# Optimization experiments

Measured on AMD Instinct MI355X. Metric: run time of the kernel, lower is better.

The kernel has to match this reference:

```python
import jax, jax.numpy as jnp
import numpy as np

N = 100000
F_IN = 128
F_OUT = 128
NNZ = 1_600_000  # avg degree 16


def spmm(rows, cols, vals, X, n):
    """Sparse [n,n] (COO: rows, cols, vals) times dense X [n,d] -> [n,d]."""
    return jax.ops.segment_sum(vals[:, None] * X[cols], rows, num_segments=n)


def setup_inputs() -> dict:
    key = jax.random.key(0)
    ks = jax.random.split(key, 8)
    x = jax.random.normal(ks[0], (N, F_IN), dtype=jnp.float32)
    W = jax.random.normal(ks[1], (F_IN, F_OUT), dtype=jnp.float32) * 0.05
    kernel = jnp.ones((N, 1), dtype=jnp.float32)  # tf.ones_initializer
    phi0_rows = jax.random.randint(ks[2], (NNZ,), 0, N, dtype=jnp.int64)
    phi0_cols = jax.random.randint(ks[3], (NNZ,), 0, N, dtype=jnp.int64)
    phi0_vals = jax.random.uniform(ks[4], (NNZ,), dtype=jnp.float32)
    phi1_rows = jax.random.randint(ks[5], (NNZ,), 0, N, dtype=jnp.int64)
    phi1_cols = jax.random.randint(ks[6], (NNZ,), 0, N, dtype=jnp.int64)
    phi1_vals = jax.random.uniform(ks[7], (NNZ,), dtype=jnp.float32)
    return {
        "x": x, "W": W, "kernel": kernel,
        "phi0_rows": phi0_rows, "phi0_cols": phi0_cols, "phi0_vals": phi0_vals,
        "phi1_rows": phi1_rows, "phi1_cols": phi1_cols, "phi1_vals": phi1_vals,
    }


def reference(x, W, kernel, phi0_rows, phi0_cols, phi0_vals,
              phi1_rows, phi1_cols, phi1_vals):
    # X' = x @ W  (dense feature projection)
    X_prime = x @ W  # [N, F_OUT]
    # X'_t = phi0 @ X'  (SpMM with wavelet basis)
    X_t = spmm(phi0_rows, phi0_cols, phi0_vals, X_prime, N)
    # out = phi1 @ (kernel * X'_t)  (elementwise spectral scaling then SpMM)
    out = spmm(phi1_rows, phi1_cols, phi1_vals, kernel * X_t, N)
    return jax.nn.relu(out)
```

## Files before the change

kernel.cpp:

```cpp
#include <hip/hip_runtime.h>


constexpr int kN = 100000;
constexpr int kF = 128;
constexpr int kNNZ = 1600000;

constexpr int kBuckets = (kN + 255) / 256;
constexpr int kBucketCap = 4608;
constexpr int kChunk = 8192;
constexpr int kChunkBlocks = (kNNZ + kChunk - 1) / kChunk;
constexpr int kScatBlocks = 2 * kChunkBlocks;
constexpr int kGemmBlocks = (kN + 63) / 64;

typedef short bf16x8 __attribute__((ext_vector_type(8)));
typedef float f32x4 __attribute__((ext_vector_type(4)));
typedef unsigned short ushort4v __attribute__((ext_vector_type(4)));

__device__ __forceinline__ unsigned short f32_to_bf16(float f) {
    unsigned int u = __float_as_uint(f);
    u += 0x7fffu + ((u >> 16) & 1u);
    return (unsigned short)(u >> 16);
}
__device__ __forceinline__ float bf16_to_f32(unsigned short h) {
    return __uint_as_float((unsigned int)h << 16);
}

__global__ __launch_bounds__(256) void transpose_w(const float* __restrict__ W,
                                                   unsigned short* __restrict__ Wt,
                                                   int* __restrict__ g0,
                                                   int* __restrict__ g1) {
    const int t = threadIdx.x;
    const int e = blockIdx.x * 256 + t;
    const int n = e & 127, k = e >> 7;
    Wt[n * 128 + k] = f32_to_bf16(W[e]);
    if (blockIdx.x == 0) {
        for (int i = t; i < kBuckets; i += 256) {
            g0[i] = i * kBucketCap;
            g1[i] = i * kBucketCap;
        }
    }
}

__global__ __launch_bounds__(256) void fused_gemm_scatter(
    const float* __restrict__ x, const unsigned short* __restrict__ Wt,
    unsigned short* __restrict__ Xpb,
    const int* __restrict__ r0, const int* __restrict__ c0, const float* __restrict__ v0,
    const int* __restrict__ r1, const int* __restrict__ c1, const float* __restrict__ v1,
    int* __restrict__ gc0, int* __restrict__ gc1,
    unsigned long long* __restrict__ s0, unsigned long long* __restrict__ s1) {
    __shared__ __align__(16) char smem[64 * 128 * 2];
    const int t = threadIdx.x;

    if (blockIdx.x >= kScatBlocks) {
        unsigned short* xs = (unsigned short*)smem;
        const int rowBase = (blockIdx.x - kScatBlocks) * 64;

        {
            const int lrow = t >> 2;
            const int q = t & 3;
            int srow = rowBase + lrow;
            if (srow >= kN) srow = kN - 1;
            const float4* xr = (const float4*)(x + (size_t)srow * kF) + q * 8;
            #pragma unroll
            for (int i = 0; i < 8; ++i) {
                const float4 f = xr[i];
                ushort4v h;
                h.x = f32_to_bf16(f.x); h.y = f32_to_bf16(f.y);
                h.z = f32_to_bf16(f.z); h.w = f32_to_bf16(f.w);
                const int kidx = q * 32 + i * 4;
                *(ushort4v*)&xs[lrow * 128 + (kidx ^ ((lrow & 7) << 3))] = h;
            }
        }
        __syncthreads();

        const int w = t >> 6;
        const int l = t & 63;
        const int lr = l & 15;
        const int lq = l >> 4;

        f32x4 acc[8];
        #pragma unroll
        for (int n = 0; n < 8; ++n) acc[n] = (f32x4){0.f, 0.f, 0.f, 0.f};

        const int arow = w * 16 + lr;
        #pragma unroll
        for (int ks = 0; ks < 4; ++ks) {
            const int akidx = ks * 32 + lq * 8;
            const bf16x8 a = *(const bf16x8*)&xs[arow * 128 + (akidx ^ ((arow & 7) << 3))];
            #pragma unroll
            for (int n = 0; n < 8; ++n) {
                const int bn = n * 16 + lr;
                const bf16x8 b = *(const bf16x8*)(Wt + bn * 128 + akidx);
                acc[n] = __builtin_amdgcn_mfma_f32_16x16x32_bf16(a, b, acc[n], 0, 0, 0);
            }
        }

        #pragma unroll
        for (int j = 0; j < 4; ++j) {
            const int row = rowBase + w * 16 + lq * 4 + j;
            if (row < kN) {
                unsigned short* orow = Xpb + (size_t)row * kF + lr;
                #pragma unroll
                for (int n = 0; n < 8; ++n) orow[n * 16] = f32_to_bf16(acc[n][j]);
            }
        }
    } else {
        int* hist = (int*)smem;
        int* hbase = hist + kBuckets;
        const int b = blockIdx.x;
        const bool m1 = b >= kChunkBlocks;
        const int cb = m1 ? b - kChunkBlocks : b;
        const int* rows = m1 ? r1 : r0;
        const int* cols = m1 ? c1 : c0;
        const float* vals = m1 ? v1 : v0;
        int* gcur = m1 ? gc1 : gc0;
        unsigned long long* stg = m1 ? s1 : s0;

        for (int i = t; i < kBuckets; i += 256) hist[i] = 0;
        __syncthreads();

        const int base0 = cb * kChunk;
        for (int j = 0; j < kChunk; j += 256) {
            const int idx = base0 + j + t;
            if (idx < kNNZ) atomicAdd(&hist[rows[idx] >> 8], 1);
        }
        __syncthreads();

        for (int i = t; i < kBuckets; i += 256) {
            const int c = hist[i];
            hbase[i] = c ? atomicAdd(&gcur[i], c) : 0;
            hist[i] = 0;
        }
        __syncthreads();

        for (int j = 0; j < kChunk; j += 256) {
            const int idx = base0 + j + t;
            if (idx < kNNZ) {
                const int r = rows[idx];
                const int bk = r >> 8;
                const int pos = hbase[bk] + atomicAdd(&hist[bk], 1);
                const unsigned int key =
                    ((unsigned int)(r & 255) << 17) | (unsigned int)cols[idx];
                stg[pos] = ((unsigned long long)__float_as_uint(vals[idx]) << 32) | key;
            }
        }
    }
}

__global__ __launch_bounds__(256) void bucket_sort(
    const int* __restrict__ gc0, const int* __restrict__ gc1,
    unsigned long long* __restrict__ s0, unsigned long long* __restrict__ s1,
    int* __restrict__ rs0, int* __restrict__ re0,
    int* __restrict__ rs1, int* __restrict__ re1) {
    __shared__ unsigned long long recs[kBucketCap];
    __shared__ int hist[256];
    __shared__ int sc[256];
    __shared__ int cur[256];

    const int b = blockIdx.x;
    const bool m1 = b >= kBuckets;
    const int bk = m1 ? b - kBuckets : b;
    const int* gcur = m1 ? gc1 : gc0;
    unsigned long long* stg = m1 ? s1 : s0;
    int* rs = m1 ? rs1 : rs0;
    int* re = m1 ? re1 : re0;

    const int t = threadIdx.x;
    const int start = bk * kBucketCap;
    const int nrec = gcur[bk] - start;

    hist[t] = 0;
    __syncthreads();

    for (int i = t; i < nrec; i += 256) {
        const unsigned long long p = stg[start + i];
        recs[i] = p;
        atomicAdd(&hist[((unsigned int)p >> 17) & 255], 1);
    }
    __syncthreads();

    const int v = hist[t];
    sc[t] = v;
    __syncthreads();
    #pragma unroll
    for (int off = 1; off < 256; off <<= 1) {
        const int add = (t >= off) ? sc[t - off] : 0;
        __syncthreads();
        sc[t] += add;
        __syncthreads();
    }
    {
        const int ex = sc[t] - v;
        cur[t] = ex;
        const int row = bk * 256 + t;
        if (row < kN) {
            rs[row] = start + ex;
            re[row] = start + sc[t];
        }
    }
    __syncthreads();

    for (int i = t; i < nrec; i += 256) {
        const unsigned long long p = recs[i];
        const int lr = (int)(((unsigned int)p >> 17) & 255);
        const int pos = atomicAdd(&cur[lr], 1);
        stg[start + pos] = p;
    }
}

template <bool ROW_SCALE, bool RELU, bool OUT_BF16>
__global__ __launch_bounds__(256) void spmm_csr(const int* __restrict__ rs,
                                                const int* __restrict__ re,
                                                const unsigned long long* __restrict__ rec,
                                                const float* __restrict__ scale,
                                                const unsigned short* __restrict__ Xin,
                                                void* __restrict__ Xout) {
    const int tid = blockIdx.x * 256 + threadIdx.x;
    const int r = tid >> 5;
    const int lane = tid & 31;

    const int s = rs[r];
    const int e = re[r];

    float4 acc = make_float4(0.f, 0.f, 0.f, 0.f);

    for (int base = s; base < e; base += 32) {
        int cl = 0;
        float vl = 0.f;
        if (base + lane < e) {
            const unsigned long long p = rec[base + lane];
            cl = (int)((unsigned int)p & 0x1FFFF);
            vl = __uint_as_float((unsigned int)(p >> 32));
        }
        const int m4 = (min(32, e - base) + 3) & ~3;
        for (int j = 0; j < m4; j += 4) {
            const int c0 = __shfl(cl, j, 32);
            const int c1 = __shfl(cl, j + 1, 32);
            const int c2 = __shfl(cl, j + 2, 32);
            const int c3 = __shfl(cl, j + 3, 32);
            const float w0 = __shfl(vl, j, 32);
            const float w1 = __shfl(vl, j + 1, 32);
            const float w2 = __shfl(vl, j + 2, 32);
            const float w3 = __shfl(vl, j + 3, 32);
            const ushort4v x0 = *(const ushort4v*)(Xin + (size_t)c0 * kF + lane * 4);
            const ushort4v x1 = *(const ushort4v*)(Xin + (size_t)c1 * kF + lane * 4);
            const ushort4v x2 = *(const ushort4v*)(Xin + (size_t)c2 * kF + lane * 4);
            const ushort4v x3 = *(const ushort4v*)(Xin + (size_t)c3 * kF + lane * 4);
            acc.x = fmaf(w0, bf16_to_f32(x0.x), acc.x);
            acc.y = fmaf(w0, bf16_to_f32(x0.y), acc.y);
            acc.z = fmaf(w0, bf16_to_f32(x0.z), acc.z);
            acc.w = fmaf(w0, bf16_to_f32(x0.w), acc.w);
            acc.x = fmaf(w1, bf16_to_f32(x1.x), acc.x);
            acc.y = fmaf(w1, bf16_to_f32(x1.y), acc.y);
            acc.z = fmaf(w1, bf16_to_f32(x1.z), acc.z);
            acc.w = fmaf(w1, bf16_to_f32(x1.w), acc.w);
            acc.x = fmaf(w2, bf16_to_f32(x2.x), acc.x);
            acc.y = fmaf(w2, bf16_to_f32(x2.y), acc.y);
            acc.z = fmaf(w2, bf16_to_f32(x2.z), acc.z);
            acc.w = fmaf(w2, bf16_to_f32(x2.w), acc.w);
            acc.x = fmaf(w3, bf16_to_f32(x3.x), acc.x);
            acc.y = fmaf(w3, bf16_to_f32(x3.y), acc.y);
            acc.z = fmaf(w3, bf16_to_f32(x3.z), acc.z);
            acc.w = fmaf(w3, bf16_to_f32(x3.w), acc.w);
        }
    }
    if (ROW_SCALE) {
        const float k = scale[r];
        acc.x *= k; acc.y *= k; acc.z *= k; acc.w *= k;
    }
    if (RELU) {
        acc.x = fmaxf(acc.x, 0.f); acc.y = fmaxf(acc.y, 0.f);
        acc.z = fmaxf(acc.z, 0.f); acc.w = fmaxf(acc.w, 0.f);
    }
    if (OUT_BF16) {
        ushort4v o;
        o.x = f32_to_bf16(acc.x); o.y = f32_to_bf16(acc.y);
        o.z = f32_to_bf16(acc.z); o.w = f32_to_bf16(acc.w);
        *(ushort4v*)((unsigned short*)Xout + (size_t)r * kF + lane * 4) = o;
    } else {
        ((float4*)Xout)[(size_t)r * 32 + lane] = acc;
    }
}

extern "C" void kernel_launch(void* const* d_in, const int* in_sizes, int n_in,
                              void* d_out, int out_size, void* d_ws, size_t ws_size,
                              hipStream_t stream) {
    const float* x    = (const float*)d_in[0];
    const float* W    = (const float*)d_in[1];
    const float* kern = (const float*)d_in[2];
    const int*   p0r  = (const int*)d_in[3];
    const int*   p0c  = (const int*)d_in[4];
    const float* p0v  = (const float*)d_in[5];
    const int*   p1r  = (const int*)d_in[6];
    const int*   p1c  = (const int*)d_in[7];
    const float* p1v  = (const float*)d_in[8];
    float* out = (float*)d_out;

    char* w = (char*)d_ws;
    size_t off = 0;
    unsigned short* Xpb = (unsigned short*)(w + off); off += (size_t)kN * kF * 2;
    unsigned short* Xtb = (unsigned short*)(w + off); off += (size_t)kN * kF * 2;
    unsigned short* Wt = (unsigned short*)(w + off);  off += 128 * 128 * 2;
    int* gcur0 = (int*)(w + off);                     off += 2048;
    int* gcur1 = (int*)(w + off);                     off += 2048;
    int* rs0 = (int*)(w + off);                       off += (size_t)kN * 4;
    int* re0 = (int*)(w + off);                       off += (size_t)kN * 4;
    int* rs1 = (int*)(w + off);                       off += (size_t)kN * 4;
    int* re1 = (int*)(w + off);                       off += (size_t)kN * 4;
    unsigned long long* stg0 = (unsigned long long*)(w + off);
    off += (size_t)kBuckets * kBucketCap * 8;
    unsigned long long* stg1 = (unsigned long long*)(w + off);
    off += (size_t)kBuckets * kBucketCap * 8;

    const int rowBlocks = kN * 32 / 256;

    transpose_w<<<64, 256, 0, stream>>>(W, Wt, gcur0, gcur1);

    fused_gemm_scatter<<<kScatBlocks + kGemmBlocks, 256, 0, stream>>>(
        x, Wt, Xpb, p0r, p0c, p0v, p1r, p1c, p1v, gcur0, gcur1, stg0, stg1);

    bucket_sort<<<2 * kBuckets, 256, 0, stream>>>(gcur0, gcur1, stg0, stg1,
                                                  rs0, re0, rs1, re1);

    spmm_csr<true, false, true><<<rowBlocks, 256, 0, stream>>>(
        rs0, re0, stg0, kern, Xpb, Xtb);

    spmm_csr<false, true, false><<<rowBlocks, 256, 0, stream>>>(
        rs1, re1, stg1, nullptr, Xtb, out);
}
```

Baseline: 206.9 us.

## Fuse per-bucket row sort into SpMM kernels with 128-row buckets

Removes the separate bucket_sort kernel and the rs/re row-pointer arrays. Each SpMM block now sorts its 128-row bucket into shared memory and consumes the records directly from LDS, so the staging array is no longer written back and re-read. Buckets shrink from 256 to 128 rows and scatter chunks from 8192 to 4096 records, and the scatter pass caches row indices in shared memory so rows are read from global memory only once. In exchange, each wave processes 16 rows serially and there are fewer, larger SpMM blocks, which may lower parallelism and latency hiding.

```diff
diff --git a/kernel.cpp b/kernel.cpp
--- a/kernel.cpp
+++ b/kernel.cpp
@@ -5,9 +5,9 @@
 constexpr int kF = 128;
 constexpr int kNNZ = 1600000;
 
-constexpr int kBuckets = (kN + 255) / 256;
-constexpr int kBucketCap = 4608;
-constexpr int kChunk = 8192;
+constexpr int kBuckets = (kN + 127) / 128;
+constexpr int kBucketCap = 2432;
+constexpr int kChunk = 4096;
 constexpr int kChunkBlocks = (kNNZ + kChunk - 1) / kChunk;
 constexpr int kScatBlocks = 2 * kChunkBlocks;
 constexpr int kGemmBlocks = (kN + 63) / 64;
@@ -48,7 +48,7 @@
     const int* __restrict__ r1, const int* __restrict__ c1, const float* __restrict__ v1,
     int* __restrict__ gc0, int* __restrict__ gc1,
     unsigned long long* __restrict__ s0, unsigned long long* __restrict__ s1) {
-    __shared__ __align__(16) char smem[64 * 128 * 2];
+    __shared__ __align__(16) char smem[kChunk * 4 + 2 * kBuckets * 4];
     const int t = threadIdx.x;
 
     if (blockIdx.x >= kScatBlocks) {
@@ -105,7 +105,8 @@
             }
         }
     } else {
-        int* hist = (int*)smem;
+        int* rowsc = (int*)smem;
+        int* hist  = rowsc + kChunk;
         int* hbase = hist + kBuckets;
         const int b = blockIdx.x;
         const bool m1 = b >= kChunkBlocks;
@@ -122,7 +123,9 @@
         const int base0 = cb * kChunk;
         for (int j = 0; j < kChunk; j += 256) {
             const int idx = base0 + j + t;
-            if (idx < kNNZ) atomicAdd(&hist[rows[idx] >> 8], 1);
+            const int r = (idx < kNNZ) ? rows[idx] : -1;
+            rowsc[j + t] = r;
+            if (r >= 0) atomicAdd(&hist[r >> 7], 1);
         }
         __syncthreads();
 
@@ -135,117 +138,91 @@
 
         for (int j = 0; j < kChunk; j += 256) {
             const int idx = base0 + j + t;
-            if (idx < kNNZ) {
-                const int r = rows[idx];
-                const int bk = r >> 8;
+            const int r = rowsc[j + t];
+            if (r >= 0) {
+                const int bk = r >> 7;
                 const int pos = hbase[bk] + atomicAdd(&hist[bk], 1);
                 const unsigned int key =
-                    ((unsigned int)(r & 255) << 17) | (unsigned int)cols[idx];
+                    ((unsigned int)(r & 127) << 17) | (unsigned int)cols[idx];
                 stg[pos] = ((unsigned long long)__float_as_uint(vals[idx]) << 32) | key;
             }
         }
     }
 }
 
-__global__ __launch_bounds__(256) void bucket_sort(
-    const int* __restrict__ gc0, const int* __restrict__ gc1,
-    unsigned long long* __restrict__ s0, unsigned long long* __restrict__ s1,
-    int* __restrict__ rs0, int* __restrict__ re0,
-    int* __restrict__ rs1, int* __restrict__ re1) {
+template <bool ROW_SCALE, bool RELU, bool OUT_BF16>
+__global__ __launch_bounds__(256) void sort_spmm(const int* __restrict__ gcur,
+                                                 const unsigned long long* __restrict__ stg,
+                                                 const float* __restrict__ scale,
+                                                 const unsigned short* __restrict__ Xin,
+                                                 void* __restrict__ Xout) {
     __shared__ unsigned long long recs[kBucketCap];
-    __shared__ int hist[256];
-    __shared__ int sc[256];
-    __shared__ int cur[256];
-
-    const int b = blockIdx.x;
-    const bool m1 = b >= kBuckets;
-    const int bk = m1 ? b - kBuckets : b;
-    const int* gcur = m1 ? gc1 : gc0;
-    unsigned long long* stg = m1 ? s1 : s0;
-    int* rs = m1 ? rs1 : rs0;
-    int* re = m1 ? re1 : re0;
-
+    __shared__ int hist[128];
+    __shared__ int sc[128];
+    __shared__ int cur[128];
+
+    const int bk = blockIdx.x;
     const int t = threadIdx.x;
     const int start = bk * kBucketCap;
     const int nrec = gcur[bk] - start;
 
-    hist[t] = 0;
+    if (t < 128) hist[t] = 0;
+    __syncthreads();
+
+    for (int i = t; i < nrec; i += 256) {
+        const unsigned int lo = (unsigned int)stg[start + i];
+        atomicAdd(&hist[(lo >> 17) & 127], 1);
+    }
+    __syncthreads();
+
+    const int v = (t < 128) ? hist[t] : 0;
+    if (t < 128) sc[t] = v;
+    __syncthreads();
+    #pragma unroll
+    for (int off = 1; off < 128; off <<= 1) {
+        const int add = (t < 128 && t >= off) ? sc[t - off] : 0;
+        __syncthreads();
+        if (t < 128) sc[t] += add;
+        __syncthreads();
+    }
+    if (t < 128) cur[t] = sc[t] - v;
     __syncthreads();
 
     for (int i = t; i < nrec; i += 256) {
         const unsigned long long p = stg[start + i];
-        recs[i] = p;
-        atomicAdd(&hist[((unsigned int)p >> 17) & 255], 1);
-    }
-    __syncthreads();
-
-    const int v = hist[t];
-    sc[t] = v;
-    __syncthreads();
-    #pragma unroll
-    for (int off = 1; off < 256; off <<= 1) {
-        const int add = (t >= off) ? sc[t - off] : 0;
-        __syncthreads();
-        sc[t] += add;
-        __syncthreads();
-    }
-    {
-        const int ex = sc[t] - v;
-        cur[t] = ex;
-        const int row = bk * 256 + t;
-        if (row < kN) {
-            rs[row] = start + ex;
-            re[row] = start + sc[t];
-        }
-    }
-    __syncthreads();
-
-    for (int i = t; i < nrec; i += 256) {
-        const unsigned long long p = recs[i];
-        const int lr = (int)(((unsigned int)p >> 17) & 255);
-        const int pos = atomicAdd(&cur[lr], 1);
-        stg[start + pos] = p;
-    }
-}
-
-template <bool ROW_SCALE, bool RELU, bool OUT_BF16>
-__global__ __launch_bounds__(256) void spmm_csr(const int* __restrict__ rs,
-                                                const int* __restrict__ re,
-                                                const unsigned long long* __restrict__ rec,
-                                                const float* __restrict__ scale,
-                                                const unsigned short* __restrict__ Xin,
-                                                void* __restrict__ Xout) {
-    const int tid = blockIdx.x * 256 + threadIdx.x;
-    const int r = tid >> 5;
-    const int lane = tid & 31;
-
-    const int s = rs[r];
-    const int e = re[r];
-
-    float4 acc = make_float4(0.f, 0.f, 0.f, 0.f);
-
-    for (int base = s; base < e; base += 32) {
-        int cl = 0;
-        float vl = 0.f;
-        if (base + lane < e) {
-            const unsigned long long p = rec[base + lane];
-            cl = (int)((unsigned int)p & 0x1FFFF);
-            vl = __uint_as_float((unsigned int)(p >> 32));
-        }
-        const int m4 = (min(32, e - base) + 3) & ~3;
-        for (int j = 0; j < m4; j += 4) {
-            const int c0 = __shfl(cl, j, 32);
-            const int c1 = __shfl(cl, j + 1, 32);
-            const int c2 = __shfl(cl, j + 2, 32);
-            const int c3 = __shfl(cl, j + 3, 32);
-            const float w0 = __shfl(vl, j, 32);
-            const float w1 = __shfl(vl, j + 1, 32);
-            const float w2 = __shfl(vl, j + 2, 32);
-            const float w3 = __shfl(vl, j + 3, 32);
-            const ushort4v x0 = *(const ushort4v*)(Xin + (size_t)c0 * kF + lane * 4);
-            const ushort4v x1 = *(const ushort4v*)(Xin + (size_t)c1 * kF + lane * 4);
-            const ushort4v x2 = *(const ushort4v*)(Xin + (size_t)c2 * kF + lane * 4);
-            const ushort4v x3 = *(const ushort4v*)(Xin + (size_t)c3 * kF + lane * 4);
+        const int lr = (int)(((unsigned int)p >> 17) & 127);
+        recs[atomicAdd(&cur[lr], 1)] = p;
+    }
+    __syncthreads();
+
+    const int rg = t >> 5;
+    const int lane = t & 31;
+    for (int i = 0; i < 16; ++i) {
+        const int lr = rg * 16 + i;
+        const int row = bk * 128 + lr;
+        if (row >= kN) continue;
+        const int e = sc[lr];
+        const int s = e - hist[lr];
+
+        float4 acc = make_float4(0.f, 0.f, 0.f, 0.f);
+        int j = s;
+        for (; j + 4 <= e; j += 4) {
+            const unsigned long long p0 = recs[j];
+            const unsigned long long p1 = recs[j + 1];
+            const unsigned long long p2 = recs[j + 2];
+            const unsigned long long p3 = recs[j + 3];
+            const int cc0 = (int)((unsigned int)p0 & 0x1FFFF);
+            const int cc1 = (int)((unsigned int)p1 & 0x1FFFF);
+            const int cc2 = (int)((unsigned int)p2 & 0x1FFFF);
+            const int cc3 = (int)((unsigned int)p3 & 0x1FFFF);
+            const float w0 = __uint_as_float((unsigned int)(p0 >> 32));
+            const float w1 = __uint_as_float((unsigned int)(p1 >> 32));
+            const float w2 = __uint_as_float((unsigned int)(p2 >> 32));
+            const float w3 = __uint_as_float((unsigned int)(p3 >> 32));
+            const ushort4v x0 = *(const ushort4v*)(Xin + (size_t)cc0 * kF + lane * 4);
+            const ushort4v x1 = *(const ushort4v*)(Xin + (size_t)cc1 * kF + lane * 4);
+            const ushort4v x2 = *(const ushort4v*)(Xin + (size_t)cc2 * kF + lane * 4);
+            const ushort4v x3 = *(const ushort4v*)(Xin + (size_t)cc3 * kF + lane * 4);
             acc.x = fmaf(w0, bf16_to_f32(x0.x), acc.x);
             acc.y = fmaf(w0, bf16_to_f32(x0.y), acc.y);
             acc.z = fmaf(w0, bf16_to_f32(x0.z), acc.z);
@@ -263,22 +240,33 @@
             acc.z = fmaf(w3, bf16_to_f32(x3.z), acc.z);
             acc.w = fmaf(w3, bf16_to_f32(x3.w), acc.w);
         }
-    }
-    if (ROW_SCALE) {
-        const float k = scale[r];
-        acc.x *= k; acc.y *= k; acc.z *= k; acc.w *= k;
-    }
-    if (RELU) {
-        acc.x = fmaxf(acc.x, 0.f); acc.y = fmaxf(acc.y, 0.f);
-        acc.z = fmaxf(acc.z, 0.f); acc.w = fmaxf(acc.w, 0.f);
-    }
-    if (OUT_BF16) {
-        ushort4v o;
-        o.x = f32_to_bf16(acc.x); o.y = f32_to_bf16(acc.y);
-        o.z = f32_to_bf16(acc.z); o.w = f32_to_bf16(acc.w);
-        *(ushort4v*)((unsigned short*)Xout + (size_t)r * kF + lane * 4) = o;
-    } else {
-        ((float4*)Xout)[(size_t)r * 32 + lane] = acc;
+        for (; j < e; ++j) {
+            const unsigned long long p = recs[j];
+            const int cc = (int)((unsigned int)p & 0x1FFFF);
+            const float wv = __uint_as_float((unsigned int)(p >> 32));
+            const ushort4v xv = *(const ushort4v*)(Xin + (size_t)cc * kF + lane * 4);
+            acc.x = fmaf(wv, bf16_to_f32(xv.x), acc.x);
+            acc.y = fmaf(wv, bf16_to_f32(xv.y), acc.y);
+            acc.z = fmaf(wv, bf16_to_f32(xv.z), acc.z);
+            acc.w = fmaf(wv, bf16_to_f32(xv.w), acc.w);
+        }
+
+        if (ROW_SCALE) {
+            const float k = scale[row];
+            acc.x *= k; acc.y *= k; acc.z *= k; acc.w *= k;
+        }
+        if (RELU) {
+            acc.x = fmaxf(acc.x, 0.f); acc.y = fmaxf(acc.y, 0.f);
+            acc.z = fmaxf(acc.z, 0.f); acc.w = fmaxf(acc.w, 0.f);
+        }
+        if (OUT_BF16) {
+            ushort4v o;
+            o.x = f32_to_bf16(acc.x); o.y = f32_to_bf16(acc.y);
+            o.z = f32_to_bf16(acc.z); o.w = f32_to_bf16(acc.w);
+            *(ushort4v*)((unsigned short*)Xout + (size_t)row * kF + lane * 4) = o;
+        } else {
+            ((float4*)Xout)[(size_t)row * 32 + lane] = acc;
+        }
     }
 }
 
@@ -301,30 +289,21 @@
     unsigned short* Xpb = (unsigned short*)(w + off); off += (size_t)kN * kF * 2;
     unsigned short* Xtb = (unsigned short*)(w + off); off += (size_t)kN * kF * 2;
     unsigned short* Wt = (unsigned short*)(w + off);  off += 128 * 128 * 2;
-    int* gcur0 = (int*)(w + off);                     off += 2048;
-    int* gcur1 = (int*)(w + off);                     off += 2048;
-    int* rs0 = (int*)(w + off);                       off += (size_t)kN * 4;
-    int* re0 = (int*)(w + off);                       off += (size_t)kN * 4;
-    int* rs1 = (int*)(w + off);                       off += (size_t)kN * 4;
-    int* re1 = (int*)(w + off);                       off += (size_t)kN * 4;
+    int* gcur0 = (int*)(w + off);                     off += 4096;
+    int* gcur1 = (int*)(w + off);                     off += 4096;
     unsigned long long* stg0 = (unsigned long long*)(w + off);
     off += (size_t)kBuckets * kBucketCap * 8;
     unsigned long long* stg1 = (unsigned long long*)(w + off);
     off += (size_t)kBuckets * kBucketCap * 8;
 
-    const int rowBlocks = kN * 32 / 256;
-
     transpose_w<<<64, 256, 0, stream>>>(W, Wt, gcur0, gcur1);
 
     fused_gemm_scatter<<<kScatBlocks + kGemmBlocks, 256, 0, stream>>>(
         x, Wt, Xpb, p0r, p0c, p0v, p1r, p1c, p1v, gcur0, gcur1, stg0, stg1);
 
-    bucket_sort<<<2 * kBuckets, 256, 0, stream>>>(gcur0, gcur1, stg0, stg1,
-                                                  rs0, re0, rs1, re1);
-
-    spmm_csr<true, false, true><<<rowBlocks, 256, 0, stream>>>(
-        rs0, re0, stg0, kern, Xpb, Xtb);
-
-    spmm_csr<false, true, false><<<rowBlocks, 256, 0, stream>>>(
-        rs1, re1, stg1, nullptr, Xtb, out);
-}
+    sort_spmm<true, false, true><<<kBuckets, 256, 0, stream>>>(
+        gcur0, stg0, kern, Xpb, Xtb);
+
+    sort_spmm<false, true, false><<<kBuckets, 256, 0, stream>>>(
+        gcur1, stg1, nullptr, Xtb, out);
+}
```

Result: slower. 224.0 us (+8.3%).
